# Performance work log

Measured on AMD Instinct MI355X. Metric: run time of the kernel, lower is better.

The kernel has to match this reference:

```python
import jax, jax.numpy as jnp
import numpy as np

N0, N1, N2 = 30000, 90000, 60000          # nodes, edges, triangles
D_IN, D_OUT, HEADS = 256, 128, 4
NNZ0, NNZ1, NNZ2 = 960000, 180000, 180000  # sparse incidence nnz


def setup_inputs() -> dict:
    key = jax.random.key(0)
    ks = jax.random.split(key, 18)
    s = 0.05
    return {
        "x0": jax.random.normal(ks[0], (N0, D_IN), dtype=jnp.float32),
        "x1": jax.random.normal(ks[1], (N1, D_IN), dtype=jnp.float32),
        "x2": jax.random.normal(ks[2], (N2, D_IN), dtype=jnp.float32),
        "rows0": jax.random.randint(ks[3], (NNZ0,), 0, N0),
        "cols0": jax.random.randint(ks[4], (NNZ0,), 0, N0),
        "rows1": jax.random.randint(ks[5], (NNZ1,), 0, N0),
        "cols1": jax.random.randint(ks[6], (NNZ1,), 0, N1),
        "rows2": jax.random.randint(ks[7], (NNZ2,), 0, N0),
        "cols2": jax.random.randint(ks[8], (NNZ2,), 0, N2),
        # per-head parameters (SATLayer_regular), stacked on leading head axis
        "W1": jax.random.normal(ks[9], (HEADS, D_IN, D_OUT), dtype=jnp.float32) * s,
        "b1": jax.random.normal(ks[10], (HEADS, D_OUT), dtype=jnp.float32) * s,
        "a1_w": jax.random.normal(ks[11], (HEADS, D_OUT), dtype=jnp.float32) * s,
        "a1_b": jax.random.normal(ks[12], (HEADS,), dtype=jnp.float32) * s,
        "a2_w": jax.random.normal(ks[13], (HEADS, D_OUT), dtype=jnp.float32) * s,
        "a2_b": jax.random.normal(ks[14], (HEADS,), dtype=jnp.float32) * s,
        "Wagg": jax.random.normal(ks[15], (HEADS, 4 * D_OUT, D_OUT), dtype=jnp.float32) * s,
        "bagg": jax.random.normal(ks[16], (HEADS, D_OUT), dtype=jnp.float32) * s,
    }


def reference(x0, x1, x2, rows0, cols0, rows1, cols1, rows2, cols2,
              W1, b1, a1_w, a1_b, a2_w, a2_b, Wagg, bagg):
    n0 = x0.shape[0]

    def sat_head(W1h, b1h, a1wh, a1bh, a2wh, a2bh, Waggh, baggh):
        # shared Linearlayer1 + ReLU applied to all simplex levels
        xi0 = jax.nn.relu(x0 @ W1h + b1h)   # [n0, d]
        xj1 = jax.nn.relu(x1 @ W1h + b1h)   # [n1, d]
        xj2 = jax.nn.relu(x2 @ W1h + b1h)   # [n2, d]
        a1 = xi0 @ a1wh + a1bh              # [n0] attention source term

        def attention_agg(xj, rows, cols):
            a2 = xj @ a2wh + a2bh                              # [nj]
            att = jax.nn.sigmoid(a1[rows] + a2[cols])          # [nnz]
            msg = att[:, None] * xj[cols]                      # [nnz, d]
            return jax.ops.segment_sum(msg, rows, num_segments=n0)

        agg0 = attention_agg(xi0, rows0, cols0)
        agg1 = attention_agg(xj1, rows1, cols1)
        agg2 = attention_agg(xj2, rows2, cols2)
        cat = jnp.concatenate([xi0, agg0, agg1, agg2], axis=1)  # [n0, 4d]
        return cat @ Waggh + baggh                              # [n0, d]

    # stack over heads, then mean (layer0_1 + torch.mean)
    outs = jax.vmap(sat_head)(W1, b1, a1_w, a1_b, a2_w, a2_b, Wagg, bagg)
    return jnp.mean(outs, axis=0)
```

## Files before the change

### kernel.cpp

```cpp
#include <hip/hip_runtime.h>

typedef __attribute__((ext_vector_type(8))) short short8;
typedef __attribute__((ext_vector_type(4))) float f32x4;
typedef unsigned short ushort_t;
typedef unsigned int uint32;

#define N0 30000
#define N1 90000
#define N2 60000
#define P0 30208
#define S1OFF 30208
#define S2OFF 120320
#define MPAD 180352
#define MT0 236
#define MT_ALL 1409
#define MT64Y 2818
#define NE0 960000
#define NE1 180000
#define NE2 180000
#define CSTRIDE 30720

__device__ __forceinline__ float bf2f(ushort_t u) {
    union { uint32 i; float f; } v; v.i = ((uint32)u) << 16; return v.f;
}
__device__ __forceinline__ ushort_t f2bf(float f) {
    union { float f; uint32 i; } v; v.f = f;
    uint32 x = v.i;
    x += ((x >> 16) & 1u) + 0x7FFFu;
    return (ushort_t)(x >> 16);
}

__global__ __launch_bounds__(256) void prep_w(const float* __restrict__ W1,
                                              const float* __restrict__ Wagg,
                                              const float* __restrict__ bagg,
                                              ushort_t* __restrict__ W1t,
                                              ushort_t* __restrict__ Wgt,
                                              ushort_t* __restrict__ WgtC,
                                              float* __restrict__ bsum) {
    int idx = blockIdx.x * blockDim.x + threadIdx.x;
    if (idx < 131072) {
        int h = idx >> 15, rem = idx & 32767, n = rem >> 8, k = rem & 255;
        W1t[idx] = f2bf(W1[((size_t)h * 256 + k) * 128 + n]);
    }
    if (idx < 196608) {
        int h = idx / 49152, rem = idx % 49152;
        int l = rem / 16384, rem2 = rem % 16384, n = rem2 >> 7, k = rem2 & 127;
        Wgt[idx] = f2bf(Wagg[((size_t)h * 512 + (l + 1) * 128 + k) * 128 + n]);
    }
    if (idx < 65536) {
        int n = idx >> 9, kk = idx & 511, h = kk >> 7, k = kk & 127;
        WgtC[idx] = f2bf(Wagg[((size_t)h * 512 + k) * 128 + n]);
    }
    if (idx < 128) {
        float s = 0.f;
        #pragma unroll
        for (int h = 0; h < 4; ++h) s += bagg[h * 128 + idx];
        bsum[idx] = s;
    }
}

__global__ __launch_bounds__(256) void csr_zero(int* __restrict__ cur) {
    int i = blockIdx.x * blockDim.x + threadIdx.x;
    if (i < 3 * CSTRIDE) cur[i] = 0;
}

__global__ __launch_bounds__(256) void csr_hist(const int* __restrict__ rows, int nE,
                                                int* __restrict__ cur) {
    int i = blockIdx.x * blockDim.x + threadIdx.x;
    if (i < nE) atomicAdd(cur + rows[i], 1);
}

__global__ __launch_bounds__(1024) void csr_scan(int* __restrict__ curA,
                                                 int* __restrict__ rowPtrA,
                                                 int nE0, int nE1, int nE2) {
    __shared__ int ssum[1024];
    const int b = blockIdx.x;
    int* cur = curA + b * CSTRIDE;
    int* rowPtr = rowPtrA + b * CSTRIDE;
    const int nE = (b == 0) ? nE0 : (b == 1 ? nE1 : nE2);
    const int t = threadIdx.x;
    const int base = t * 30;
    int loc[30];
    int s = 0;
    #pragma unroll
    for (int i = 0; i < 30; ++i) {
        int r = base + i;
        int v = (r < N0) ? cur[r] : 0;
        loc[i] = s; s += v;
    }
    ssum[t] = s;
    __syncthreads();
    for (int off = 1; off < 1024; off <<= 1) {
        int v = (t >= off) ? ssum[t - off] : 0;
        __syncthreads();
        ssum[t] += v;
        __syncthreads();
    }
    int carry = (t == 0) ? 0 : ssum[t - 1];
    #pragma unroll
    for (int i = 0; i < 30; ++i) {
        int r = base + i;
        if (r < N0) {
            int p = carry + loc[i];
            rowPtr[r] = p;
            cur[r] = p;
        }
    }
    if (t == 0) rowPtr[N0] = nE;
}

__global__ __launch_bounds__(256) void csr_scatter(const int* __restrict__ rows,
                                                   const int* __restrict__ cols,
                                                   int nE, int Sl,
                                                   int* __restrict__ cur,
                                                   int* __restrict__ sortedCg) {
    int i = blockIdx.x * blockDim.x + threadIdx.x;
    if (i < nE) {
        int pos = atomicAdd(cur + rows[i], 1);
        sortedCg[pos] = Sl + cols[i];
    }
}

__global__ __launch_bounds__(256, 3)
void gemm_y(const float* __restrict__ x0, const float* __restrict__ x1,
            const float* __restrict__ x2,
            const ushort_t* __restrict__ W1t, const float* __restrict__ b1,
            ushort_t* __restrict__ Y)
{
    __shared__ ushort_t As[64 * 256];
    __shared__ ushort_t Bs[2][128 * 40];
    const int tid = threadIdx.x;
    const int lane = tid & 63;
    const int wn = tid >> 6;
    const int l15 = lane & 15, lg = lane >> 4;
    const int r0 = blockIdx.x * 64;

    const float* src; int jbase, nreal;
    if (r0 < P0)          { src = x0; jbase = r0;         nreal = N0; }
    else if (r0 < S2OFF)  { src = x1; jbase = r0 - S1OFF; nreal = N1; }
    else                  { src = x2; jbase = r0 - S2OFF; nreal = N2; }

    #pragma unroll
    for (int p = 0; p < 8; ++p) {
        int chunk = tid + p * 256;
        int row = chunk >> 5, c = chunk & 31;
        int j = jbase + row;
        ushort_t o[8] __attribute__((aligned(16)));
        if (j < nreal) {
            const float4 v0 = *(const float4*)(src + (size_t)j * 256 + c * 8);
            const float4 v1 = *(const float4*)(src + (size_t)j * 256 + c * 8 + 4);
            o[0] = f2bf(v0.x); o[1] = f2bf(v0.y); o[2] = f2bf(v0.z); o[3] = f2bf(v0.w);
            o[4] = f2bf(v1.x); o[5] = f2bf(v1.y); o[6] = f2bf(v1.z); o[7] = f2bf(v1.w);
        } else {
            #pragma unroll
            for (int i = 0; i < 8; ++i) o[i] = 0;
        }
        *(uint4*)(As + row * 256 + ((c ^ (row & 7)) << 3)) = *(const uint4*)o;
    }

    const int hh = wn >> 1;
    const int nbase = (wn & 1) * 64;

    #pragma unroll 1
    for (int hp = 0; hp < 2; ++hp) {
        f32x4 acc[4][4] = {};
        #pragma unroll 1
        for (int kt = 0; kt < 256; kt += 32) {
            __syncthreads();
            #pragma unroll
            for (int q = 0; q < 4; ++q) {
                int id = tid + q * 256;
                int bh = id >> 9, rem = id & 511;
                int n = rem >> 2, c = rem & 3;
                *(uint4*)(Bs[bh] + n * 40 + c * 8) =
                    *(const uint4*)(W1t + (hp * 2 + bh) * 32768 + n * 256 + kt + c * 8);
            }
            __syncthreads();

            short8 af[4], bf[4];
            #pragma unroll
            for (int m = 0; m < 4; ++m) {
                int row = m * 16 + l15;
                af[m] = *(const short8*)(As + row * 256 + ((((kt >> 3) + lg) ^ (row & 7)) << 3));
            }
            #pragma unroll
            for (int nf = 0; nf < 4; ++nf) {
                int nrow = nbase + nf * 16 + l15;
                bf[nf] = *(const short8*)(Bs[hh] + nrow * 40 + lg * 8);
            }
            #pragma unroll
            for (int m = 0; m < 4; ++m)
                #pragma unroll
                for (int nf = 0; nf < 4; ++nf)
                    acc[m][nf] = __builtin_amdgcn_mfma_f32_16x16x32_bf16(af[m], bf[nf], acc[m][nf], 0, 0, 0);
        }
        int h = hp * 2 + hh;
        #pragma unroll
        for (int nf = 0; nf < 4; ++nf) {
            int col = nbase + nf * 16 + l15;
            float bb = b1[h * 128 + col];
            #pragma unroll
            for (int m = 0; m < 4; ++m)
            #pragma unroll
            for (int j = 0; j < 4; ++j) {
                int row = r0 + m * 16 + lg * 4 + j;
                float v = acc[m][nf][j] + bb;
                v = v > 0.f ? v : 0.f;
                Y[(size_t)row * 512 + h * 128 + col] = f2bf(v);
            }
        }
    }
}

__global__ __launch_bounds__(256) void gemm_z(ushort_t* Y,
                                              const ushort_t* __restrict__ Wgt,
                                              const float* __restrict__ a1w,
                                              const float* __restrict__ a1b,
                                              const float* __restrict__ a2w,
                                              const float* __restrict__ a2b,
                                              float* __restrict__ a1o,
                                              float* __restrict__ a2o) {
    __shared__ ushort_t As[128 * 136];
    __shared__ ushort_t Bs[128 * 136];
    __shared__ float a1wS[128], a2wS[128];
    const int tid = threadIdx.x;
    const int h = blockIdx.y;
    const int r0 = blockIdx.x * 128;
    const int l = (r0 < P0) ? 0 : (r0 < S2OFF ? 1 : 2);
    const ushort_t* B = Wgt + ((h * 3 + l) << 14);
    ushort_t* A = Y + (size_t)h * 128;

    if (tid < 128) {
        a1wS[tid] = a1w[h * 128 + tid];
        a2wS[tid] = a2w[h * 128 + tid];
    }
    #pragma unroll
    for (int c = 0; c < 8; ++c) {
        int idx = tid + c * 256;
        int row = idx >> 4, ch = idx & 15;
        *(uint4*)(As + row * 136 + ch * 8) =
            *(const uint4*)(A + (size_t)(r0 + row) * 512 + ch * 8);
        *(uint4*)(Bs + row * 136 + ch * 8) = *(const uint4*)(B + row * 128 + ch * 8);
    }
    __syncthreads();

    {
        int row = tid >> 1, half = tid & 1;
        const ushort_t* yr = As + row * 136 + half * 64;
        float d1 = 0.f, d2 = 0.f;
        #pragma unroll
        for (int t = 0; t < 8; ++t) {
            short8 v = *(const short8*)(yr + t * 8);
            #pragma unroll
            for (int j = 0; j < 8; ++j) {
                float f = bf2f(((const ushort_t*)&v)[j]);
                d2 += f * a2wS[half * 64 + t * 8 + j];
                d1 += f * a1wS[half * 64 + t * 8 + j];
            }
        }
        d2 += __shfl_xor(d2, 1);
        d1 += __shfl_xor(d1, 1);
        if (half == 0) {
            a2o[(size_t)h * MPAD + r0 + row] = d2 + a2b[h];
            if (l == 0) a1o[(size_t)h * P0 + r0 + row] = d1 + a1b[h];
        }
    }

    const int lane = tid & 63;
    const int wid = tid >> 6;
    const int wm = wid >> 1, wn = wid & 1;
    const int l15 = lane & 15, lg = lane >> 4;

    f32x4 acc[4][4] = {};
    #pragma unroll
    for (int kt = 0; kt < 128; kt += 32) {
        short8 af[4], bfr[4];
        #pragma unroll
        for (int m = 0; m < 4; ++m)
            af[m] = *(const short8*)(As + (wm * 64 + m * 16 + l15) * 136 + kt + lg * 8);
        #pragma unroll
        for (int n = 0; n < 4; ++n)
            bfr[n] = *(const short8*)(Bs + (wn * 64 + n * 16 + l15) * 136 + kt + lg * 8);
        #pragma unroll
        for (int m = 0; m < 4; ++m)
            #pragma unroll
            for (int n = 0; n < 4; ++n)
                acc[m][n] = __builtin_amdgcn_mfma_f32_16x16x32_bf16(af[m], bfr[n], acc[m][n], 0, 0, 0);
    }

    #pragma unroll
    for (int m = 0; m < 4; ++m)
    #pragma unroll
    for (int n = 0; n < 4; ++n)
    #pragma unroll
    for (int j = 0; j < 4; ++j) {
        int row = r0 + wm * 64 + m * 16 + lg * 4 + j;
        int col = wn * 64 + n * 16 + l15;
        A[(size_t)row * 512 + col] = f2bf(acc[m][n][j]);
    }
}

__global__ __launch_bounds__(256)
void gemm_init(const ushort_t* __restrict__ A,
               const ushort_t* __restrict__ B,
               float* __restrict__ outF,
               const float* __restrict__ bias)
{
    __shared__ ushort_t As[128 * 40];
    __shared__ ushort_t Bs[128 * 40];
    const int tid = threadIdx.x;
    const int lane = tid & 63;
    const int wid = tid >> 6;
    const int wm = wid >> 1, wn = wid & 1;
    const int r0 = blockIdx.x * 128;
    const int l15 = lane & 15, lg = lane >> 4;

    f32x4 acc[4][4] = {};

    for (int kt = 0; kt < 512; kt += 32) {
        #pragma unroll
        for (int c = 0; c < 2; ++c) {
            int idx = tid + c * 256;
            int row = idx >> 2, kc = idx & 3;
            uint4 va = *(const uint4*)(A + (size_t)(r0 + row) * 512 + kt + kc * 8);
            *(uint4*)(As + row * 40 + kc * 8) = va;
            uint4 vb = *(const uint4*)(B + (size_t)row * 512 + kt + kc * 8);
            *(uint4*)(Bs + row * 40 + kc * 8) = vb;
        }
        __syncthreads();
        short8 af[4], bfr[4];
        #pragma unroll
        for (int m = 0; m < 4; ++m)
            af[m] = *(const short8*)(As + (wm * 64 + m * 16 + l15) * 40 + lg * 8);
        #pragma unroll
        for (int n = 0; n < 4; ++n)
            bfr[n] = *(const short8*)(Bs + (wn * 64 + n * 16 + l15) * 40 + lg * 8);
        #pragma unroll
        for (int m = 0; m < 4; ++m)
            #pragma unroll
            for (int n = 0; n < 4; ++n)
                acc[m][n] = __builtin_amdgcn_mfma_f32_16x16x32_bf16(af[m], bfr[n], acc[m][n], 0, 0, 0);
        __syncthreads();
    }

    #pragma unroll
    for (int m = 0; m < 4; ++m)
    #pragma unroll
    for (int n = 0; n < 4; ++n)
    #pragma unroll
    for (int j = 0; j < 4; ++j) {
        int row = r0 + wm * 64 + m * 16 + lg * 4 + j;
        int col = wn * 64 + n * 16 + l15;
        if (row < N0) outF[(size_t)row * 128 + col] = 0.25f * (acc[m][n][j] + bias[col]);
    }
}

__global__ __launch_bounds__(256) void pull_agg(const int* __restrict__ rowPtr,
                                                const int* __restrict__ sortedCg,
                                                const float* __restrict__ a1,
                                                const float* __restrict__ a2,
                                                const ushort_t* __restrict__ z,
                                                float* __restrict__ out) {
    int w = blockIdx.x * 4 + (threadIdx.x >> 6);
    if (w >= N0) return;
    const int lane = threadIdx.x & 63;
    const int h = lane >> 4, g = lane & 15;

    const float a1r = a1[(size_t)h * P0 + w];
    const float* a2h = a2 + (size_t)h * MPAD;
    int beg = rowPtr[w], end = rowPtr[w + 1];

    float acc[8] = {0.f, 0.f, 0.f, 0.f, 0.f, 0.f, 0.f, 0.f};
    int e = beg;
    int n4 = beg + ((end - beg) & ~3);
    for (; e < n4; e += 4) {
        int cg0 = sortedCg[e],     cg1 = sortedCg[e + 1];
        int cg2 = sortedCg[e + 2], cg3 = sortedCg[e + 3];
        float att0 = 0.25f / (1.f + __expf(-(a1r + a2h[cg0])));
        float att1 = 0.25f / (1.f + __expf(-(a1r + a2h[cg1])));
        float att2 = 0.25f / (1.f + __expf(-(a1r + a2h[cg2])));
        float att3 = 0.25f / (1.f + __expf(-(a1r + a2h[cg3])));
        uint4 v0 = *(const uint4*)(z + (size_t)cg0 * 512 + lane * 8);
        uint4 v1 = *(const uint4*)(z + (size_t)cg1 * 512 + lane * 8);
        uint4 v2 = *(const uint4*)(z + (size_t)cg2 * 512 + lane * 8);
        uint4 v3 = *(const uint4*)(z + (size_t)cg3 * 512 + lane * 8);
        const ushort_t* u0 = (const ushort_t*)&v0;
        const ushort_t* u1 = (const ushort_t*)&v1;
        const ushort_t* u2 = (const ushort_t*)&v2;
        const ushort_t* u3 = (const ushort_t*)&v3;
        #pragma unroll
        for (int j = 0; j < 8; ++j)
            acc[j] += att0 * bf2f(u0[j]) + att1 * bf2f(u1[j])
                    + att2 * bf2f(u2[j]) + att3 * bf2f(u3[j]);
    }
    for (; e < end; ++e) {
        int cg = sortedCg[e];
        float att = 0.25f / (1.f + __expf(-(a1r + a2h[cg])));
        uint4 v = *(const uint4*)(z + (size_t)cg * 512 + lane * 8);
        const ushort_t* u = (const ushort_t*)&v;
        #pragma unroll
        for (int j = 0; j < 8; ++j) acc[j] += att * bf2f(u[j]);
    }
    #pragma unroll
    for (int j = 0; j < 8; ++j) {
        acc[j] += __shfl_xor(acc[j], 16);
        acc[j] += __shfl_xor(acc[j], 32);
    }
    float2* p = (float2*)(out + (size_t)w * 128 + g * 8 + h * 2);
    float2 o = *p;
    o.x += acc[h * 2 + 0];
    o.y += acc[h * 2 + 1];
    *p = o;
}

extern "C" void kernel_launch(void* const* d_in, const int* in_sizes, int n_in,
                              void* d_out, int out_size, void* d_ws, size_t ws_size,
                              hipStream_t stream) {
    const float* x0   = (const float*)d_in[0];
    const float* x1   = (const float*)d_in[1];
    const float* x2   = (const float*)d_in[2];
    const int* rows0  = (const int*)d_in[3];
    const int* cols0  = (const int*)d_in[4];
    const int* rows1  = (const int*)d_in[5];
    const int* cols1  = (const int*)d_in[6];
    const int* rows2  = (const int*)d_in[7];
    const int* cols2  = (const int*)d_in[8];
    const float* W1   = (const float*)d_in[9];
    const float* b1   = (const float*)d_in[10];
    const float* a1w  = (const float*)d_in[11];
    const float* a1b  = (const float*)d_in[12];
    const float* a2w  = (const float*)d_in[13];
    const float* a2b  = (const float*)d_in[14];
    const float* Wagg = (const float*)d_in[15];
    const float* bagg = (const float*)d_in[16];
    float* out = (float*)d_out;
    char* ws = (char*)d_ws;

    ushort_t* Y      = (ushort_t*)(ws);
    float*    a1o    = (float*)(ws + 184680448);
    float*    a2o    = (float*)(ws + 185163776);
    ushort_t* W1t    = (ushort_t*)(ws + 188049408);
    ushort_t* Wgt    = (ushort_t*)(ws + 188311552);
    ushort_t* WgtC   = (ushort_t*)(ws + 188704768);
    float*    bsum   = (float*)(ws + 188835840);
    int*      cur    = (int*)(ws + 188836352);
    int*      rowPtr = (int*)(ws + 189204992);
    int*      srtCg  = (int*)(ws + 189573632);

    int* cur0 = cur,    * cur1 = cur + CSTRIDE,    * cur2 = cur + 2 * CSTRIDE;
    int* rp0  = rowPtr, * rp1  = rowPtr + CSTRIDE, * rp2  = rowPtr + 2 * CSTRIDE;
    int* srt0 = srtCg,  * srt1 = srtCg + NE0,      * srt2 = srtCg + NE0 + NE1;

    csr_zero<<<(3 * CSTRIDE + 255) / 256, 256, 0, stream>>>(cur);
    csr_hist<<<(NE0 + 255) / 256, 256, 0, stream>>>(rows0, NE0, cur0);
    csr_hist<<<(NE1 + 255) / 256, 256, 0, stream>>>(rows1, NE1, cur1);
    csr_hist<<<(NE2 + 255) / 256, 256, 0, stream>>>(rows2, NE2, cur2);
    csr_scan<<<3, 1024, 0, stream>>>(cur, rowPtr, NE0, NE1, NE2);
    csr_scatter<<<(NE0 + 255) / 256, 256, 0, stream>>>(rows0, cols0, NE0, 0,     cur0, srt0);
    csr_scatter<<<(NE1 + 255) / 256, 256, 0, stream>>>(rows1, cols1, NE1, S1OFF, cur1, srt1);
    csr_scatter<<<(NE2 + 255) / 256, 256, 0, stream>>>(rows2, cols2, NE2, S2OFF, cur2, srt2);

    prep_w<<<768, 256, 0, stream>>>(W1, Wagg, bagg, W1t, Wgt, WgtC, bsum);
    gemm_y<<<MT64Y, 256, 0, stream>>>(x0, x1, x2, W1t, b1, Y);

    gemm_init<<<MT0, 256, 0, stream>>>(Y, WgtC, out, bsum);

    gemm_z<<<dim3(MT_ALL, 4), 256, 0, stream>>>(Y, Wgt, a1w, a1b, a2w, a2b, a1o, a2o);

    pull_agg<<<(N0 + 3) / 4, 256, 0, stream>>>(rp0, srt0, a1o, a2o, Y, out);
    pull_agg<<<(N0 + 3) / 4, 256, 0, stream>>>(rp1, srt1, a1o, a2o, Y, out);
    pull_agg<<<(N0 + 3) / 4, 256, 0, stream>>>(rp2, srt2, a1o, a2o, Y, out);
}
```

Measured before the change: 622.0 us.

## Fuse edge/triangle feature GEMM with Wagg projection and merge CSR build launches

Levels 1 and 2 (edges and triangles) now go through a new fused kernel. It computes relu(x@W1+b1) into shared memory, takes the a2 attention dot product there, and multiplies directly by the per-level Wagg slice to write the projected Z into the Y buffer. This removes the round trip of writing and re-reading the intermediate Y for those rows, which are most of the rows, and gemm_z now runs only over the level-0 tiles. The three histogram and three scatter launches are also merged into single kernels to cut launch overhead. In exchange, each fused block does both GEMM stages sequentially with extra syncs and lower per-block parallelism.

```diff
diff --git a/kernel.cpp b/kernel.cpp
--- a/kernel.cpp
+++ b/kernel.cpp
@@ -14,10 +14,12 @@
 #define MPAD 180352
 #define MT0 236
 #define MT_ALL 1409
-#define MT64Y 2818
+#define L0B 472
+#define FZB 2346
 #define NE0 960000
 #define NE1 180000
 #define NE2 180000
+#define NNZ_ALL 1320000
 #define CSTRIDE 30720
 
 __device__ __forceinline__ float bf2f(ushort_t u) {
@@ -64,10 +66,14 @@
     if (i < 3 * CSTRIDE) cur[i] = 0;
 }
 
-__global__ __launch_bounds__(256) void csr_hist(const int* __restrict__ rows, int nE,
-                                                int* __restrict__ cur) {
+__global__ __launch_bounds__(256) void csr_hist_all(const int* __restrict__ rows0,
+                                                    const int* __restrict__ rows1,
+                                                    const int* __restrict__ rows2,
+                                                    int* __restrict__ cur) {
     int i = blockIdx.x * blockDim.x + threadIdx.x;
-    if (i < nE) atomicAdd(cur + rows[i], 1);
+    if (i < NE0)                 atomicAdd(cur + rows0[i], 1);
+    else if (i < NE0 + NE1)      atomicAdd(cur + CSTRIDE + rows1[i - NE0], 1);
+    else if (i < NNZ_ALL)        atomicAdd(cur + 2 * CSTRIDE + rows2[i - NE0 - NE1], 1);
 }
 
 __global__ __launch_bounds__(1024) void csr_scan(int* __restrict__ curA,
@@ -109,15 +115,26 @@
     if (t == 0) rowPtr[N0] = nE;
 }
 
-__global__ __launch_bounds__(256) void csr_scatter(const int* __restrict__ rows,
-                                                   const int* __restrict__ cols,
-                                                   int nE, int Sl,
-                                                   int* __restrict__ cur,
-                                                   int* __restrict__ sortedCg) {
+__global__ __launch_bounds__(256) void csr_scatter_all(const int* __restrict__ rows0,
+                                                       const int* __restrict__ cols0,
+                                                       const int* __restrict__ rows1,
+                                                       const int* __restrict__ cols1,
+                                                       const int* __restrict__ rows2,
+                                                       const int* __restrict__ cols2,
+                                                       int* __restrict__ cur,
+                                                       int* __restrict__ srtCg) {
     int i = blockIdx.x * blockDim.x + threadIdx.x;
-    if (i < nE) {
-        int pos = atomicAdd(cur + rows[i], 1);
-        sortedCg[pos] = Sl + cols[i];
+    if (i < NE0) {
+        int pos = atomicAdd(cur + rows0[i], 1);
+        srtCg[pos] = cols0[i];
+    } else if (i < NE0 + NE1) {
+        int j = i - NE0;
+        int pos = atomicAdd(cur + CSTRIDE + rows1[j], 1);
+        srtCg[NE0 + pos] = S1OFF + cols1[j];
+    } else if (i < NNZ_ALL) {
+        int j = i - NE0 - NE1;
+        int pos = atomicAdd(cur + 2 * CSTRIDE + rows2[j], 1);
+        srtCg[NE0 + NE1 + pos] = S2OFF + cols2[j];
     }
 }
 
@@ -207,6 +224,165 @@
                 float v = acc[m][nf][j] + bb;
                 v = v > 0.f ? v : 0.f;
                 Y[(size_t)row * 512 + h * 128 + col] = f2bf(v);
+            }
+        }
+    }
+}
+
+__global__ __launch_bounds__(256)
+void gemm_y_fz(const float* __restrict__ x1, const float* __restrict__ x2,
+               const ushort_t* __restrict__ W1t, const float* __restrict__ b1,
+               const float* __restrict__ a2w, const float* __restrict__ a2b,
+               const ushort_t* __restrict__ Wgt,
+               float* __restrict__ a2o, ushort_t* __restrict__ Z)
+{
+    __shared__ ushort_t As[64 * 256];
+    __shared__ ushort_t Bs[2][128 * 40];
+    __shared__ ushort_t Ys[64 * 128];
+    const int tid = threadIdx.x;
+    const int lane = tid & 63;
+    const int wn = tid >> 6;
+    const int l15 = lane & 15, lg = lane >> 4;
+    const int r0 = (L0B + blockIdx.x) * 64;
+    const int l = (r0 < S2OFF) ? 1 : 2;
+    const float* src = (l == 1) ? x1 : x2;
+    const int jbase = r0 - ((l == 1) ? S1OFF : S2OFF);
+    const int nreal = (l == 1) ? N1 : N2;
+
+    #pragma unroll
+    for (int p = 0; p < 8; ++p) {
+        int chunk = tid + p * 256;
+        int row = chunk >> 5, c = chunk & 31;
+        int j = jbase + row;
+        ushort_t o[8] __attribute__((aligned(16)));
+        if (j < nreal) {
+            const float4 v0 = *(const float4*)(src + (size_t)j * 256 + c * 8);
+            const float4 v1 = *(const float4*)(src + (size_t)j * 256 + c * 8 + 4);
+            o[0] = f2bf(v0.x); o[1] = f2bf(v0.y); o[2] = f2bf(v0.z); o[3] = f2bf(v0.w);
+            o[4] = f2bf(v1.x); o[5] = f2bf(v1.y); o[6] = f2bf(v1.z); o[7] = f2bf(v1.w);
+        } else {
+            #pragma unroll
+            for (int i = 0; i < 8; ++i) o[i] = 0;
+        }
+        *(uint4*)(As + row * 256 + ((c ^ (row & 7)) << 3)) = *(const uint4*)o;
+    }
+
+    const int hh = wn >> 1;
+    const int nbase = (wn & 1) * 64;
+    const int wm2 = wn >> 1, wn2 = wn & 1;
+
+    #pragma unroll 1
+    for (int hp = 0; hp < 2; ++hp) {
+        f32x4 acc[4][4] = {};
+        #pragma unroll 1
+        for (int kt = 0; kt < 256; kt += 32) {
+            __syncthreads();
+            #pragma unroll
+            for (int q = 0; q < 4; ++q) {
+                int id = tid + q * 256;
+                int bh = id >> 9, rem = id & 511;
+                int n = rem >> 2, c = rem & 3;
+                *(uint4*)(Bs[bh] + n * 40 + c * 8) =
+                    *(const uint4*)(W1t + (hp * 2 + bh) * 32768 + n * 256 + kt + c * 8);
+            }
+            __syncthreads();
+
+            short8 af[4], bf[4];
+            #pragma unroll
+            for (int m = 0; m < 4; ++m) {
+                int row = m * 16 + l15;
+                af[m] = *(const short8*)(As + row * 256 + ((((kt >> 3) + lg) ^ (row & 7)) << 3));
+            }
+            #pragma unroll
+            for (int nf = 0; nf < 4; ++nf) {
+                int nrow = nbase + nf * 16 + l15;
+                bf[nf] = *(const short8*)(Bs[hh] + nrow * 40 + lg * 8);
+            }
+            #pragma unroll
+            for (int m = 0; m < 4; ++m)
+                #pragma unroll
+                for (int nf = 0; nf < 4; ++nf)
+                    acc[m][nf] = __builtin_amdgcn_mfma_f32_16x16x32_bf16(af[m], bf[nf], acc[m][nf], 0, 0, 0);
+        }
+
+        #pragma unroll 1
+        for (int sub = 0; sub < 2; ++sub) {
+            const int h = hp * 2 + sub;
+            __syncthreads();
+            if (hh == sub) {
+                #pragma unroll
+                for (int nf = 0; nf < 4; ++nf) {
+                    int col = nbase + nf * 16 + l15;
+                    float bb = b1[h * 128 + col];
+                    #pragma unroll
+                    for (int m = 0; m < 4; ++m)
+                    #pragma unroll
+                    for (int j = 0; j < 4; ++j) {
+                        int row = m * 16 + lg * 4 + j;
+                        float v = acc[m][nf][j] + bb;
+                        v = v > 0.f ? v : 0.f;
+                        int c = col >> 3;
+                        Ys[row * 128 + ((c ^ (row & 7)) << 3) + (col & 7)] = f2bf(v);
+                    }
+                }
+            }
+            __syncthreads();
+
+            {
+                int row = tid >> 2, q = tid & 3;
+                float d2 = 0.f;
+                #pragma unroll
+                for (int i = 0; i < 4; ++i) {
+                    int c = q * 4 + i;
+                    short8 v = *(const short8*)(Ys + row * 128 + ((c ^ (row & 7)) << 3));
+                    #pragma unroll
+                    for (int jj = 0; jj < 8; ++jj)
+                        d2 += bf2f(((const ushort_t*)&v)[jj]) * a2w[h * 128 + c * 8 + jj];
+                }
+                d2 += __shfl_xor(d2, 1);
+                d2 += __shfl_xor(d2, 2);
+                if (q == 0) a2o[(size_t)h * MPAD + r0 + row] = d2 + a2b[h];
+            }
+
+            const ushort_t* Bz = Wgt + ((h * 3 + l) << 14);
+            f32x4 zacc[2][4] = {};
+            #pragma unroll 1
+            for (int kt2 = 0; kt2 < 4; ++kt2) {
+                __syncthreads();
+                #pragma unroll
+                for (int q2 = 0; q2 < 2; ++q2) {
+                    int id = tid + q2 * 256;
+                    int brow = id >> 2, cc = id & 3;
+                    *(uint4*)(Bs[0] + brow * 40 + cc * 8) =
+                        *(const uint4*)(Bz + brow * 128 + kt2 * 32 + cc * 8);
+                }
+                __syncthreads();
+                short8 af2[2], bf2[4];
+                #pragma unroll
+                for (int m = 0; m < 2; ++m) {
+                    int row = wm2 * 32 + m * 16 + l15;
+                    af2[m] = *(const short8*)(Ys + row * 128 + (((kt2 * 4 + lg) ^ (row & 7)) << 3));
+                }
+                #pragma unroll
+                for (int n = 0; n < 4; ++n) {
+                    int nrow = wn2 * 64 + n * 16 + l15;
+                    bf2[n] = *(const short8*)(Bs[0] + nrow * 40 + lg * 8);
+                }
+                #pragma unroll
+                for (int m = 0; m < 2; ++m)
+                    #pragma unroll
+                    for (int n = 0; n < 4; ++n)
+                        zacc[m][n] = __builtin_amdgcn_mfma_f32_16x16x32_bf16(af2[m], bf2[n], zacc[m][n], 0, 0, 0);
+            }
+            #pragma unroll
+            for (int m = 0; m < 2; ++m)
+            #pragma unroll
+            for (int n = 0; n < 4; ++n)
+            #pragma unroll
+            for (int j = 0; j < 4; ++j) {
+                int row = r0 + wm2 * 32 + m * 16 + lg * 4 + j;
+                int col = wn2 * 64 + n * 16 + l15;
+                Z[(size_t)row * 512 + h * 128 + col] = f2bf(zacc[m][n][j]);
             }
         }
     }
@@ -226,7 +402,7 @@
     const int tid = threadIdx.x;
     const int h = blockIdx.y;
     const int r0 = blockIdx.x * 128;
-    const int l = (r0 < P0) ? 0 : (r0 < S2OFF ? 1 : 2);
+    const int l = 0;
     const ushort_t* B = Wgt + ((h * 3 + l) << 14);
     ushort_t* A = Y + (size_t)h * 128;
 
@@ -262,7 +438,7 @@
         d1 += __shfl_xor(d1, 1);
         if (half == 0) {
             a2o[(size_t)h * MPAD + r0 + row] = d2 + a2b[h];
-            if (l == 0) a1o[(size_t)h * P0 + r0 + row] = d1 + a1b[h];
+            a1o[(size_t)h * P0 + r0 + row] = d1 + a1b[h];
         }
     }
 
@@ -447,25 +623,22 @@
     int*      rowPtr = (int*)(ws + 189204992);
     int*      srtCg  = (int*)(ws + 189573632);
 
-    int* cur0 = cur,    * cur1 = cur + CSTRIDE,    * cur2 = cur + 2 * CSTRIDE;
     int* rp0  = rowPtr, * rp1  = rowPtr + CSTRIDE, * rp2  = rowPtr + 2 * CSTRIDE;
     int* srt0 = srtCg,  * srt1 = srtCg + NE0,      * srt2 = srtCg + NE0 + NE1;
 
     csr_zero<<<(3 * CSTRIDE + 255) / 256, 256, 0, stream>>>(cur);
-    csr_hist<<<(NE0 + 255) / 256, 256, 0, stream>>>(rows0, NE0, cur0);
-    csr_hist<<<(NE1 + 255) / 256, 256, 0, stream>>>(rows1, NE1, cur1);
-    csr_hist<<<(NE2 + 255) / 256, 256, 0, stream>>>(rows2, NE2, cur2);
+    csr_hist_all<<<(NNZ_ALL + 255) / 256, 256, 0, stream>>>(rows0, rows1, rows2, cur);
     csr_scan<<<3, 1024, 0, stream>>>(cur, rowPtr, NE0, NE1, NE2);
-    csr_scatter<<<(NE0 + 255) / 256, 256, 0, stream>>>(rows0, cols0, NE0, 0,     cur0, srt0);
-    csr_scatter<<<(NE1 + 255) / 256, 256, 0, stream>>>(rows1, cols1, NE1, S1OFF, cur1, srt1);
-    csr_scatter<<<(NE2 + 255) / 256, 256, 0, stream>>>(rows2, cols2, NE2, S2OFF, cur2, srt2);
+    csr_scatter_all<<<(NNZ_ALL + 255) / 256, 256, 0, stream>>>(
+        rows0, cols0, rows1, cols1, rows2, cols2, cur, srtCg);
 
     prep_w<<<768, 256, 0, stream>>>(W1, Wagg, bagg, W1t, Wgt, WgtC, bsum);
-    gemm_y<<<MT64Y, 256, 0, stream>>>(x0, x1, x2, W1t, b1, Y);
+    gemm_y<<<L0B, 256, 0, stream>>>(x0, x1, x2, W1t, b1, Y);
+    gemm_y_fz<<<FZB, 256, 0, stream>>>(x1, x2, W1t, b1, a2w, a2b, Wgt, a2o, Y);
 
     gemm_init<<<MT0, 256, 0, stream>>>(Y, WgtC, out, bsum);
 
-    gemm_z<<<dim3(MT_ALL, 4), 256, 0, stream>>>(Y, Wgt, a1w, a1b, a2w, a2b, a1o, a2o);
+    gemm_z<<<dim3(MT0, 4), 256, 0, stream>>>(Y, Wgt, a1w, a1b, a2w, a2b, a1o, a2o);
 
     pull_agg<<<(N0 + 3) / 4, 256, 0, stream>>>(rp0, srt0, a1o, a2o, Y, out);
     pull_agg<<<(N0 + 3) / 4, 256, 0, stream>>>(rp1, srt1, a1o, a2o, Y, out);
```

Result: slower. 821.1 us (+32.0%).
